# Kernel optimization log

Measured on AMD Instinct MI355X. Metric: run time of the kernel, lower is better.

## Reference

```python
import jax, jax.numpy as jnp
import numpy as np

N, C, E, G = 100000, 200, 400000, 512
H, D = 4, 50  # heads, per-head dim (out_channels // num_heads)
NEG_SLOPE = 0.2
EPS_LN = 1e-5


def setup_inputs() -> dict:
    key = jax.random.key(0)
    ks = jax.random.split(key, 12)
    x = jax.random.normal(ks[0], (N, C), dtype=jnp.float32)
    edge_index = jax.random.randint(ks[1], (2, E), 0, N, dtype=jnp.int64)
    batch = jnp.sort(jax.random.randint(ks[2], (N,), 0, G, dtype=jnp.int64))
    # LayerNorm (graph mode) affine params
    ln_w = jnp.ones((C,), jnp.float32)
    ln_b = jnp.zeros((C,), jnp.float32)
    # GATConv params: W [C, H*D], att_src/att_dst [H, D], bias [H*D]
    s = 1.0 / np.sqrt(C)
    W_gat = jax.random.uniform(ks[3], (C, H * D), jnp.float32, -s, s)
    att_src = jax.random.uniform(ks[4], (H, D), jnp.float32, -s, s)
    att_dst = jax.random.uniform(ks[5], (H, D), jnp.float32, -s, s)
    bias_gat = jnp.zeros((H * D,), jnp.float32)
    # SAGPooling scoring GraphConv(C -> 1): lin_rel (with bias) + lin_root (no bias)
    w_rel = jax.random.uniform(ks[6], (C, 1), jnp.float32, -s, s)
    b_rel = jnp.zeros((1,), jnp.float32)
    w_root = jax.random.uniform(ks[7], (C, 1), jnp.float32, -s, s)
    return {"x": x, "edge_index": edge_index, "batch": batch,
            "ln_w": ln_w, "ln_b": ln_b, "W_gat": W_gat, "att_src": att_src,
            "att_dst": att_dst, "bias_gat": bias_gat,
            "w_rel": w_rel, "b_rel": b_rel, "w_root": w_root}


def reference(x, edge_index, batch, ln_w, ln_b, W_gat, att_src, att_dst,
              bias_gat, w_rel, b_rel, w_root):
    n = x.shape[0]
    # --- PyG LayerNorm, mode='graph': normalize over all nodes+channels per graph
    cnt = jax.ops.segment_sum(jnp.ones((n,), x.dtype), batch, G)          # [G]
    denom = cnt * C
    mean = jax.ops.segment_sum(x.sum(-1), batch, G) / denom               # [G]
    ex2 = jax.ops.segment_sum((x * x).sum(-1), batch, G) / denom          # [G]
    var = ex2 - mean * mean
    h = (x - mean[batch, None]) * jax.lax.rsqrt(var + EPS_LN)[batch, None]
    h = h * ln_w + ln_b
    h = jax.nn.elu(h)
    # --- GATConv (concat heads, self-loops added, eval-mode dropout)
    loops = jnp.arange(n, dtype=edge_index.dtype)
    src = jnp.concatenate([edge_index[0], loops])                          # [E+N]
    dst = jnp.concatenate([edge_index[1], loops])
    xh = (h @ W_gat).reshape(n, H, D)                                      # [N,H,D]
    a_src = (xh * att_src).sum(-1)                                         # [N,H]
    a_dst = (xh * att_dst).sum(-1)
    alpha = jax.nn.leaky_relu(a_src[src] + a_dst[dst], NEG_SLOPE)          # [E+N,H]
    m = jax.ops.segment_max(alpha, dst, n)                                 # segment softmax
    e = jnp.exp(alpha - m[dst])
    z = jax.ops.segment_sum(e, dst, n)
    att = e / (z[dst] + 1e-16)
    out = jax.ops.segment_sum(xh[src] * att[:, :, None], dst, n)           # [N,H,D]
    out = out.reshape(n, H * D) + bias_gat                                 # [N,C]
    # --- SAGPooling(min_score=-1): GraphConv score -> per-graph softmax -> multiply
    agg = jax.ops.segment_sum(out[edge_index[0]], edge_index[1], n)        # neighbor sum
    score = (agg @ w_rel + b_rel + out @ w_root)[:, 0]                     # [N]
    sm = score - jax.ops.segment_max(score, batch, G)[batch]
    es = jnp.exp(sm)
    score = es / jax.ops.segment_sum(es, batch, G)[batch]
    # softmax scores in (0,1) > min_score=-1 -> all nodes kept, x scaled by score
    xp = out * score[:, None]                                              # [N,C]
    # --- global_add_pool
    g = jax.ops.segment_sum(xp, batch, G)                                  # [G,C]
    return (xp, g)
```

## Files before the change

### kernel.cpp

```cpp
#include <hip/hip_runtime.h>
#include <hip/hip_bf16.h>

#define NN 100000
#define CC 200
#define EE 400000
#define GG 512

typedef __bf16 bf16x8 __attribute__((ext_vector_type(8)));
typedef float f32x4 __attribute__((ext_vector_type(4)));

__device__ __forceinline__ float bfraw(unsigned int u) { return __uint_as_float(u << 16); }
__device__ __forceinline__ unsigned short f2bfraw(float f) {
  __hip_bfloat16 b = __float2bfloat16(f);
  union { __hip_bfloat16 b; unsigned short u; } cv; cv.b = b; return cv.u;
}
__device__ __forceinline__ float hsel(float4 v, int h) {
  return h == 0 ? v.x : h == 1 ? v.y : h == 2 ? v.z : v.w;
}

__global__ void k_detect(const unsigned int* __restrict__ lnw_raw,
                         const unsigned int* __restrict__ ei_raw, int* __restrict__ flags) {
  if (threadIdx.x == 0 && blockIdx.x == 0) {
    flags[0] = (lnw_raw[0] == 0x3F800000u) ? 1 : 0;
    flags[1] = (ei_raw[1] == 0u && ei_raw[3] == 0u && ei_raw[5] == 0u && ei_raw[7] == 0u) ? 1 : 0;
  }
}

__global__ void k_cvt_edges(const int* __restrict__ raw, const int* __restrict__ flags,
                            int* __restrict__ out, int* __restrict__ deg) {
  int i = blockIdx.x * 256 + threadIdx.x;
  if (i >= 2 * EE) return;
  int v = flags[1] ? raw[2 * i] : raw[i];
  out[i] = v;
  if (i >= EE) atomicAdd(&deg[v], 1);
}

__global__ void k_cvt_params(const void* lnw, const void* lnb, const void* W,
                             const void* attS, const void* attD, const void* bias,
                             const void* wrel, const void* brel, const void* wroot,
                             const int* __restrict__ flags, unsigned short* __restrict__ out) {
  int i = blockIdx.x * 256 + threadIdx.x;
  if (i > 41400) return;
  const void* p; int off;
  if (i < 200)        { p = lnw;  off = i; }
  else if (i < 400)   { p = lnb;  off = i - 200; }
  else if (i < 40400) { p = W;    off = i - 400; }
  else if (i < 40600) { p = attS; off = i - 40400; }
  else if (i < 40800) { p = attD; off = i - 40600; }
  else if (i < 41000) { p = bias; off = i - 40800; }
  else if (i < 41200) { p = wrel; off = i - 41000; }
  else if (i < 41400) { p = wroot; off = i - 41200; }
  else                { p = brel; off = 0; }
  out[i] = flags[0] ? f2bfraw(((const float*)p)[off]) : ((const unsigned short*)p)[off];
}

__global__ void k_batch(const int* __restrict__ raw, const int* __restrict__ flags,
                        int* __restrict__ batch, int* __restrict__ starts) {
  int i = blockIdx.x * 256 + threadIdx.x;
  if (i >= NN) return;
  int f = flags[1];
  int b = f ? raw[2 * i] : raw[i];
  batch[i] = b;
  int pb = (i == 0) ? -1 : (f ? raw[2 * i - 2] : raw[i - 1]);
  for (int g = pb + 1; g <= b; ++g) starts[g] = i;
  if (i == NN - 1) {
    for (int g = b + 1; g <= GG; ++g) starts[g] = NN;
  }
}

__global__ void k_ln_stats(const void* __restrict__ x, const int* __restrict__ starts,
                           const int* __restrict__ flags, float* __restrict__ gacc) {
  __shared__ float sh1[4], sh2[4];
  int g = blockIdx.x >> 3, chunk = blockIdx.x & 7;
  int r0 = starts[g], r1 = starts[g + 1], cnt = r1 - r0;
  int ra = r0 + (cnt * chunk) / 8;
  int rb = r0 + (cnt * (chunk + 1)) / 8;
  float s1 = 0.f, s2 = 0.f;
  if (flags[0]) {
    const float4* xv = (const float4*)x;
    for (int i = ra * 50 + (int)threadIdx.x; i < rb * 50; i += 256) {
      float4 r = xv[i];
      s1 += r.x + r.y + r.z + r.w;
      s2 += r.x * r.x + r.y * r.y + r.z * r.z + r.w * r.w;
    }
  } else {
    const uint4* xv = (const uint4*)x;
    for (int i = ra * 25 + (int)threadIdx.x; i < rb * 25; i += 256) {
      uint4 r = xv[i];
      unsigned int w[4] = {r.x, r.y, r.z, r.w};
#pragma unroll
      for (int j = 0; j < 4; ++j) {
        float a = bfraw(w[j] & 0xffffu);
        float b = bfraw(w[j] >> 16);
        s1 += a + b; s2 += a * a + b * b;
      }
    }
  }
#pragma unroll
  for (int o = 32; o > 0; o >>= 1) { s1 += __shfl_down(s1, o, 64); s2 += __shfl_down(s2, o, 64); }
  if ((threadIdx.x & 63) == 0) { sh1[threadIdx.x >> 6] = s1; sh2[threadIdx.x >> 6] = s2; }
  __syncthreads();
  if (threadIdx.x == 0) {
    atomicAdd(&gacc[g * 2],     sh1[0] + sh1[1] + sh1[2] + sh1[3]);
    atomicAdd(&gacc[g * 2 + 1], sh2[0] + sh2[1] + sh2[2] + sh2[3]);
  }
}

__global__ void k_ln_fin(const float* __restrict__ gacc, const int* __restrict__ starts,
                         float* __restrict__ mean, float* __restrict__ rstd) {
  int g = blockIdx.x * 64 + threadIdx.x;
  if (g >= GG) return;
  int cnt = starts[g + 1] - starts[g];
  if (cnt > 0) {
    float denom = (float)cnt * (float)CC;
    float m = gacc[g * 2] / denom;
    float var = gacc[g * 2 + 1] / denom - m * m;
    mean[g] = m;
    rstd[g] = rsqrtf(var + 1e-5f);
  } else { mean[g] = 0.f; rstd[g] = 0.f; }
}

__global__ void k_wpack(const unsigned short* __restrict__ W, unsigned short* __restrict__ wp) {
  int idx = blockIdx.x * 256 + threadIdx.x;
  if (idx >= 13 * 7 * 64 * 8) return;
  int j = idx & 7;
  int rest = idx >> 3;
  int l = rest & 63;
  int ts = rest >> 6;
  int s = ts % 7, t = ts / 7;
  int k = s * 32 + (l >> 4) * 8 + j;
  int n = t * 16 + (l & 15);
  wp[idx] = (k < CC && n < CC) ? W[k * CC + n] : (unsigned short)0;
}

__global__ void k_ngemm(const void* __restrict__ x, const int* __restrict__ batch,
                        const float* __restrict__ mean, const float* __restrict__ rstd,
                        const unsigned short* __restrict__ lnw, const unsigned short* __restrict__ lnb,
                        const unsigned short* __restrict__ attS, const unsigned short* __restrict__ attD,
                        const unsigned short* __restrict__ wp, const int* __restrict__ flags,
                        unsigned short* __restrict__ xh,
                        float* __restrict__ asrc, float* __restrict__ adst) {
  int gw = (blockIdx.x * 256 + threadIdx.x) >> 6;
  int lane = threadIdx.x & 63;
  int mbase = gw * 16;
  if (mbase >= NN) return;
  int quad = lane >> 4, l15 = lane & 15;
  int row = mbase + l15;
  int b = batch[row];
  float m = mean[b], rs = rstd[b];
  bool f32in = flags[0] != 0;
  f32x4 acc[13];
#pragma unroll
  for (int t = 0; t < 13; ++t) { f32x4 zz = {0.f, 0.f, 0.f, 0.f}; acc[t] = zz; }
  const bf16x8* wv = (const bf16x8*)wp;
#pragma unroll
  for (int s = 0; s < 7; ++s) {
    int kb = s * 32 + quad * 8;
    union { bf16x8 v; unsigned short u[8]; unsigned int w[4]; } af;
    if (kb < CC) {
      float v[8];
      if (f32in) {
        const float* xp = (const float*)x + (size_t)row * CC + kb;
        float4 a = *(const float4*)xp, c = *(const float4*)(xp + 4);
        v[0]=a.x; v[1]=a.y; v[2]=a.z; v[3]=a.w; v[4]=c.x; v[5]=c.y; v[6]=c.z; v[7]=c.w;
      } else {
        uint4 r = *(const uint4*)((const unsigned short*)x + (size_t)row * CC + kb);
        unsigned int w[4] = {r.x, r.y, r.z, r.w};
#pragma unroll
        for (int j = 0; j < 4; ++j) { v[2*j] = bfraw(w[j] & 0xffffu); v[2*j+1] = bfraw(w[j] >> 16); }
      }
      uint4 wv4 = *(const uint4*)(lnw + kb);
      uint4 bv4 = *(const uint4*)(lnb + kb);
      unsigned int ww[4] = {wv4.x, wv4.y, wv4.z, wv4.w};
      unsigned int bb[4] = {bv4.x, bv4.y, bv4.z, bv4.w};
#pragma unroll
      for (int j = 0; j < 4; ++j) {
        float t0 = (v[2*j]   - m) * rs * bfraw(ww[j] & 0xffffu) + bfraw(bb[j] & 0xffffu);
        float t1 = (v[2*j+1] - m) * rs * bfraw(ww[j] >> 16)     + bfraw(bb[j] >> 16);
        t0 = t0 > 0.f ? t0 : __expf(t0) - 1.f;
        t1 = t1 > 0.f ? t1 : __expf(t1) - 1.f;
        af.u[2*j]   = f2bfraw(t0);
        af.u[2*j+1] = f2bfraw(t1);
      }
    } else {
#pragma unroll
      for (int j = 0; j < 4; ++j) af.w[j] = 0u;
    }
#pragma unroll
    for (int t = 0; t < 13; ++t) {
      bf16x8 bf = wv[(t * 7 + s) * 64 + lane];
      acc[t] = __builtin_amdgcn_mfma_f32_16x16x32_bf16(af.v, bf, acc[t], 0, 0, 0);
    }
  }
#pragma unroll
  for (int t = 0; t < 13; ++t) {
    int c = t * 16 + l15;
    if (c < CC) {
#pragma unroll
      for (int r = 0; r < 4; ++r) {
        int mrow = mbase + quad * 4 + r;
        xh[(size_t)mrow * CC + c] = f2bfraw(acc[t][r]);
      }
    }
  }
  float wsv[13], wdv[13]; int hv[13];
#pragma unroll
  for (int t = 0; t < 13; ++t) {
    int c = t * 16 + l15;
    bool ok = c < CC;
    hv[t]  = ok ? c / 50 : 0;
    wsv[t] = ok ? bfraw(attS[ok ? c : 0]) : 0.f;
    wdv[t] = ok ? bfraw(attD[ok ? c : 0]) : 0.f;
  }
#pragma unroll
  for (int r = 0; r < 4; ++r) {
    float ps[4] = {0.f, 0.f, 0.f, 0.f}, pd[4] = {0.f, 0.f, 0.f, 0.f};
#pragma unroll
    for (int t = 0; t < 13; ++t) {
      float v = acc[t][r];
      float fs = v * wsv[t], fd = v * wdv[t];
#pragma unroll
      for (int j = 0; j < 4; ++j) {
        ps[j] += (hv[t] == j) ? fs : 0.f;
        pd[j] += (hv[t] == j) ? fd : 0.f;
      }
    }
#pragma unroll
    for (int mm = 1; mm < 16; mm <<= 1) {
#pragma unroll
      for (int j = 0; j < 4; ++j) {
        ps[j] += __shfl_xor(ps[j], mm, 64);
        pd[j] += __shfl_xor(pd[j], mm, 64);
      }
    }
    if (l15 == 0) {
      int rw = mbase + quad * 4 + r;
      *(float4*)(asrc + (size_t)rw * 4) = make_float4(ps[0], ps[1], ps[2], ps[3]);
      *(float4*)(adst + (size_t)rw * 4) = make_float4(pd[0], pd[1], pd[2], pd[3]);
    }
  }
}

__global__ void k_scan1(const int* __restrict__ deg, int* __restrict__ rowptr, int* __restrict__ sums) {
  __shared__ int sh[256];
  int tid = threadIdx.x;
  int base = blockIdx.x * 1024 + tid * 4;
  int v[4]; int s = 0;
#pragma unroll
  for (int j = 0; j < 4; ++j) { int i = base + j; v[j] = (i < NN) ? deg[i] : 0; s += v[j]; }
  sh[tid] = s;
  __syncthreads();
  for (int o = 1; o < 256; o <<= 1) {
    int t = (tid >= o) ? sh[tid - o] : 0;
    __syncthreads();
    sh[tid] += t;
    __syncthreads();
  }
  int run = sh[tid] - s;
#pragma unroll
  for (int j = 0; j < 4; ++j) { int i = base + j; if (i < NN) rowptr[i] = run; run += v[j]; }
  if (tid == 255) sums[blockIdx.x] = sh[255];
}

__global__ void k_scan2(int* __restrict__ sums, int nb) {
  __shared__ int sh[128];
  int tid = threadIdx.x;
  int v = (tid < nb) ? sums[tid] : 0;
  sh[tid] = v;
  __syncthreads();
  for (int o = 1; o < 128; o <<= 1) {
    int t = (tid >= o) ? sh[tid - o] : 0;
    __syncthreads();
    sh[tid] += t;
    __syncthreads();
  }
  if (tid < nb) sums[tid] = sh[tid] - v;
}

__global__ void k_scan3(int* __restrict__ rowptr, const int* __restrict__ sums) {
  int tid = threadIdx.x;
  int add = sums[blockIdx.x];
  int base = blockIdx.x * 1024 + tid * 4;
#pragma unroll
  for (int j = 0; j < 4; ++j) { int i = base + j; if (i < NN) rowptr[i] += add; }
  if (blockIdx.x == 0 && tid == 0) rowptr[NN] = EE;
}

__global__ void k_scatter(const int* __restrict__ ei32, const int* __restrict__ rowptr,
                          int* __restrict__ fill, int* __restrict__ csrc) {
  int e = blockIdx.x * 256 + threadIdx.x;
  if (e >= EE) return;
  int s = ei32[e], d = ei32[EE + e];
  int pos = rowptr[d] + atomicAdd(&fill[d], 1);
  csrc[pos] = s;
}

__global__ void k_out(const unsigned short* __restrict__ xh, const float* __restrict__ asrc,
                      const float* __restrict__ adst,
                      const int* __restrict__ rowptr, const int* __restrict__ csrc,
                      const unsigned short* __restrict__ bias, const unsigned short* __restrict__ wrel,
                      const unsigned short* __restrict__ wroot,
                      unsigned short* __restrict__ out,
                      float* __restrict__ srel, float* __restrict__ sroot) {
  __shared__ float sA[256], sB[256];
  int tid = threadIdx.x;
  int local = tid / 25;
  int sub = tid - local * 25;
  int n = blockIdx.x * 10 + local;
  bool active = (local < 10) && (n < NN);
  float pr = 0.f, pq = 0.f;
  if (active) {
    int c0 = sub * 8;
    int hh0 = c0 / 50;
    int hh1 = hh0 < 3 ? hh0 + 1 : hh0;
    int bnd = (hh0 + 1) * 50;
    bool cr[8];
#pragma unroll
    for (int j = 0; j < 8; ++j) cr[j] = (c0 + j) >= bnd;
    float4 adn = *(const float4*)(adst + (size_t)n * 4);
    float4 asn = *(const float4*)(asrc + (size_t)n * 4);
    float ad_lo = hsel(adn, hh0), ad_hi = hsel(adn, hh1);
    float al_lo = hsel(asn, hh0) + ad_lo;
    float al_hi = hsel(asn, hh1) + ad_hi;
    al_lo = al_lo > 0.f ? al_lo : 0.2f * al_lo;
    al_hi = al_hi > 0.f ? al_hi : 0.2f * al_hi;
    float e_lo = __expf(al_lo), e_hi = __expf(al_hi);
    float z_lo = e_lo, z_hi = e_hi;
    float acc[8];
    {
      uint4 xv = *(const uint4*)(xh + (size_t)n * CC + c0);
      unsigned int w[4] = {xv.x, xv.y, xv.z, xv.w};
#pragma unroll
      for (int j = 0; j < 4; ++j) {
        float lo = bfraw(w[j] & 0xffffu), hi = bfraw(w[j] >> 16);
        acc[2*j]   = (cr[2*j]   ? e_hi : e_lo) * lo;
        acc[2*j+1] = (cr[2*j+1] ? e_hi : e_lo) * hi;
      }
    }
    int p0 = rowptr[n], p1 = rowptr[n + 1];
    int p = p0;
    for (; p + 2 <= p1; p += 2) {
      int s0 = csrc[p], s1 = csrc[p + 1];
      uint4 g0 = *(const uint4*)(xh + (size_t)s0 * CC + c0);
      uint4 g1 = *(const uint4*)(xh + (size_t)s1 * CC + c0);
      float4 av0 = *(const float4*)(asrc + (size_t)s0 * 4);
      float4 av1 = *(const float4*)(asrc + (size_t)s1 * 4);
      float b0lo = hsel(av0, hh0) + ad_lo, b0hi = hsel(av0, hh1) + ad_hi;
      float b1lo = hsel(av1, hh0) + ad_lo, b1hi = hsel(av1, hh1) + ad_hi;
      b0lo = b0lo > 0.f ? b0lo : 0.2f * b0lo;
      b0hi = b0hi > 0.f ? b0hi : 0.2f * b0hi;
      b1lo = b1lo > 0.f ? b1lo : 0.2f * b1lo;
      b1hi = b1hi > 0.f ? b1hi : 0.2f * b1hi;
      float a0lo = __expf(b0lo), a0hi = __expf(b0hi);
      float a1lo = __expf(b1lo), a1hi = __expf(b1hi);
      z_lo += a0lo + a1lo; z_hi += a0hi + a1hi;
      unsigned int w0[4] = {g0.x, g0.y, g0.z, g0.w};
      unsigned int w1[4] = {g1.x, g1.y, g1.z, g1.w};
#pragma unroll
      for (int j = 0; j < 4; ++j) {
        acc[2*j]   += (cr[2*j]   ? a0hi : a0lo) * bfraw(w0[j] & 0xffffu);
        acc[2*j+1] += (cr[2*j+1] ? a0hi : a0lo) * bfraw(w0[j] >> 16);
      }
#pragma unroll
      for (int j = 0; j < 4; ++j) {
        acc[2*j]   += (cr[2*j]   ? a1hi : a1lo) * bfraw(w1[j] & 0xffffu);
        acc[2*j+1] += (cr[2*j+1] ? a1hi : a1lo) * bfraw(w1[j] >> 16);
      }
    }
    if (p < p1) {
      int s0 = csrc[p];
      uint4 g0 = *(const uint4*)(xh + (size_t)s0 * CC + c0);
      float4 av0 = *(const float4*)(asrc + (size_t)s0 * 4);
      float b0lo = hsel(av0, hh0) + ad_lo, b0hi = hsel(av0, hh1) + ad_hi;
      b0lo = b0lo > 0.f ? b0lo : 0.2f * b0lo;
      b0hi = b0hi > 0.f ? b0hi : 0.2f * b0hi;
      float a0lo = __expf(b0lo), a0hi = __expf(b0hi);
      z_lo += a0lo; z_hi += a0hi;
      unsigned int w0[4] = {g0.x, g0.y, g0.z, g0.w};
#pragma unroll
      for (int j = 0; j < 4; ++j) {
        acc[2*j]   += (cr[2*j]   ? a0hi : a0lo) * bfraw(w0[j] & 0xffffu);
        acc[2*j+1] += (cr[2*j+1] ? a0hi : a0lo) * bfraw(w0[j] >> 16);
      }
    }
    float rz_lo = 1.f / (z_lo + 1e-16f);
    float rz_hi = 1.f / (z_hi + 1e-16f);
    uint4 bv = *(const uint4*)(bias + c0);
    uint4 rv = *(const uint4*)(wrel + c0);
    uint4 qv = *(const uint4*)(wroot + c0);
    unsigned int bw[4] = {bv.x, bv.y, bv.z, bv.w};
    unsigned int rw[4] = {rv.x, rv.y, rv.z, rv.w};
    unsigned int qw[4] = {qv.x, qv.y, qv.z, qv.w};
    unsigned int ow[4];
#pragma unroll
    for (int j = 0; j < 4; ++j) {
      float v0 = acc[2*j]   * (cr[2*j]   ? rz_hi : rz_lo) + bfraw(bw[j] & 0xffffu);
      float v1 = acc[2*j+1] * (cr[2*j+1] ? rz_hi : rz_lo) + bfraw(bw[j] >> 16);
      ow[j] = (unsigned int)f2bfraw(v0) | ((unsigned int)f2bfraw(v1) << 16);
      pr += v0 * bfraw(rw[j] & 0xffffu) + v1 * bfraw(rw[j] >> 16);
      pq += v0 * bfraw(qw[j] & 0xffffu) + v1 * bfraw(qw[j] >> 16);
    }
    *(uint4*)(out + (size_t)n * CC + c0) = make_uint4(ow[0], ow[1], ow[2], ow[3]);
  }
  sA[tid] = pr; sB[tid] = pq;
  __syncthreads();
  if (active && sub == 0) {
    float a = 0.f, b = 0.f;
#pragma unroll
    for (int k = 0; k < 25; ++k) { a += sA[tid + k]; b += sB[tid + k]; }
    srel[n] = a; sroot[n] = b;
  }
}

__global__ void k_score(const float* __restrict__ srel, const float* __restrict__ sroot,
                        const unsigned short* __restrict__ brel, const int* __restrict__ rowptr,
                        const int* __restrict__ csrc, float* __restrict__ score) {
  int n = blockIdx.x * 256 + threadIdx.x;
  if (n >= NN) return;
  float sc = bfraw(brel[0]) + sroot[n];
  int p0 = rowptr[n], p1 = rowptr[n + 1];
  int p = p0;
  float s0 = 0.f, s1 = 0.f;
  for (; p + 2 <= p1; p += 2) { s0 += srel[csrc[p]]; s1 += srel[csrc[p + 1]]; }
  if (p < p1) s0 += srel[csrc[p]];
  score[n] = sc + s0 + s1;
}

__global__ void k_gsoftmax(const float* __restrict__ score, const int* __restrict__ starts,
                           float* __restrict__ smax, float* __restrict__ ssum) {
  __shared__ float sh[4];
  __shared__ float bc;
  int g = blockIdx.x;
  int r0 = starts[g], r1 = starts[g + 1];
  float m = -3.0e38f;
  for (int i = r0 + (int)threadIdx.x; i < r1; i += 256) m = fmaxf(m, score[i]);
#pragma unroll
  for (int o = 32; o > 0; o >>= 1) m = fmaxf(m, __shfl_down(m, o, 64));
  if ((threadIdx.x & 63) == 0) sh[threadIdx.x >> 6] = m;
  __syncthreads();
  if (threadIdx.x == 0) bc = fmaxf(fmaxf(sh[0], sh[1]), fmaxf(sh[2], sh[3]));
  __syncthreads();
  float mm = bc;
  float s = 0.f;
  for (int i = r0 + (int)threadIdx.x; i < r1; i += 256) s += expf(score[i] - mm);
#pragma unroll
  for (int o = 32; o > 0; o >>= 1) s += __shfl_down(s, o, 64);
  if ((threadIdx.x & 63) == 0) sh[threadIdx.x >> 6] = s;
  __syncthreads();
  if (threadIdx.x == 0) { smax[g] = mm; ssum[g] = sh[0] + sh[1] + sh[2] + sh[3]; }
}

__global__ void k_xpg(const unsigned short* __restrict__ out, const float* __restrict__ score,
                      const float* __restrict__ smax, const float* __restrict__ ssum,
                      const int* __restrict__ starts, const int* __restrict__ flags,
                      void* __restrict__ dout, float* __restrict__ gsum) {
  __shared__ float part[10][200];
  int g = blockIdx.x >> 3, chunk = blockIdx.x & 7;
  int r0 = starts[g], r1 = starts[g + 1], cnt = r1 - r0;
  int ra = r0 + (cnt * chunk) / 8;
  int rb = r0 + (cnt * (chunk + 1)) / 8;
  int tid = threadIdx.x;
  int rg = tid / 25, sub = tid - rg * 25;
  int f32o = flags[0];
  float sm = smax[g], si = ssum[g];
  float rsi = (si > 0.f) ? 1.f / si : 0.f;
  if (rg < 10) {
    float acc[8];
#pragma unroll
    for (int j = 0; j < 8; ++j) acc[j] = 0.f;
    for (int r = ra + rg; r < rb; r += 10) {
      float sf = __expf(score[r] - sm) * rsi;
      uint4 xv = *(const uint4*)(out + (size_t)r * CC + sub * 8);
      unsigned int w[4] = {xv.x, xv.y, xv.z, xv.w};
      float v[8];
#pragma unroll
      for (int j = 0; j < 4; ++j) {
        v[2*j]   = bfraw(w[j] & 0xffffu) * sf;
        v[2*j+1] = bfraw(w[j] >> 16) * sf;
        acc[2*j] += v[2*j]; acc[2*j+1] += v[2*j+1];
      }
      if (f32o) {
        float* dp = (float*)dout + (size_t)r * CC + sub * 8;
        *(float4*)dp       = make_float4(v[0], v[1], v[2], v[3]);
        *(float4*)(dp + 4) = make_float4(v[4], v[5], v[6], v[7]);
      } else {
        unsigned int o[4];
#pragma unroll
        for (int j = 0; j < 4; ++j)
          o[j] = (unsigned int)f2bfraw(v[2*j]) | ((unsigned int)f2bfraw(v[2*j+1]) << 16);
        *(uint4*)((unsigned short*)dout + (size_t)r * CC + sub * 8) = make_uint4(o[0], o[1], o[2], o[3]);
      }
    }
#pragma unroll
    for (int j = 0; j < 8; ++j) part[rg][sub * 8 + j] = acc[j];
  }
  __syncthreads();
  if (tid < 200) {
    float s = 0.f;
#pragma unroll
    for (int k = 0; k < 10; ++k) s += part[k][tid];
    atomicAdd(&gsum[g * 200 + tid], s);
  }
}

__global__ void k_gfin(const float* __restrict__ gsum, const int* __restrict__ flags,
                       void* __restrict__ dout) {
  int i = blockIdx.x * 256 + threadIdx.x;
  if (i >= GG * 200) return;
  float s = gsum[i];
  size_t o = (size_t)NN * CC + i;
  if (flags[0]) ((float*)dout)[o] = s;
  else ((unsigned short*)dout)[o] = f2bfraw(s);
}

constexpr size_t O_FLAGS  = 0;
constexpr size_t O_STARTS = 16;
constexpr size_t O_MEAN   = 2080;
constexpr size_t O_RSTD   = 4128;
constexpr size_t O_SMAX   = 6176;
constexpr size_t O_SSUM   = 8224;
constexpr size_t O_SUMS   = 10272;
constexpr size_t O_PAR    = 10784;
constexpr size_t O_WPACK  = 93600;
constexpr size_t O_BATCH  = 186784;
constexpr size_t O_EI32   = 586784;
constexpr size_t O_DEG    = 3786784;
constexpr size_t O_FILL   = 4186784;
constexpr size_t O_ROWPTR = 4586784;
constexpr size_t O_CSRC   = 4986912;
constexpr size_t O_ASRC   = 6586912;
constexpr size_t O_ADST   = 8186912;
constexpr size_t O_SREL   = 9786912;
constexpr size_t O_SROOT  = 10186912;
constexpr size_t O_SCORE  = 10586912;
constexpr size_t O_GACC   = 10986912;
constexpr size_t O_GSUM   = 10991008;
constexpr size_t O_XH     = 11400608;
constexpr size_t O_OUT    = 51400608;

extern "C" void kernel_launch(void* const* d_in, const int* in_sizes, int n_in,
                              void* d_out, int out_size, void* d_ws, size_t ws_size,
                              hipStream_t stream) {
  const void* x     = d_in[0];
  const int*  ei    = (const int*)d_in[1];
  const int*  batchr= (const int*)d_in[2];
  const void* lnw_r = d_in[3];
  const void* lnb_r = d_in[4];
  const void* Wg_r  = d_in[5];
  const void* attS_r= d_in[6];
  const void* attD_r= d_in[7];
  const void* bias_r= d_in[8];
  const void* wrel_r= d_in[9];
  const void* brel_r= d_in[10];
  const void* wroot_r=d_in[11];

  char* ws = (char*)d_ws;
  int*   flags  = (int*)(ws + O_FLAGS);
  int*   starts = (int*)(ws + O_STARTS);
  float* mean   = (float*)(ws + O_MEAN);
  float* rstd   = (float*)(ws + O_RSTD);
  float* smax   = (float*)(ws + O_SMAX);
  float* ssum   = (float*)(ws + O_SSUM);
  int*   sums   = (int*)(ws + O_SUMS);
  unsigned short* par = (unsigned short*)(ws + O_PAR);
  unsigned short* wpack = (unsigned short*)(ws + O_WPACK);
  int*   batch  = (int*)(ws + O_BATCH);
  int*   ei32   = (int*)(ws + O_EI32);
  int*   deg    = (int*)(ws + O_DEG);
  int*   fill   = (int*)(ws + O_FILL);
  int*   rowptr = (int*)(ws + O_ROWPTR);
  int*   csrc   = (int*)(ws + O_CSRC);
  float* asrc   = (float*)(ws + O_ASRC);
  float* adst   = (float*)(ws + O_ADST);
  float* srel   = (float*)(ws + O_SREL);
  float* sroot  = (float*)(ws + O_SROOT);
  float* score  = (float*)(ws + O_SCORE);
  float* gacc   = (float*)(ws + O_GACC);
  float* gsum   = (float*)(ws + O_GSUM);
  unsigned short* xh    = (unsigned short*)(ws + O_XH);
  unsigned short* outws = (unsigned short*)(ws + O_OUT);

  unsigned short* lnw  = par;
  unsigned short* lnb  = par + 200;
  unsigned short* Wc   = par + 400;
  unsigned short* attS = par + 40400;
  unsigned short* attD = par + 40600;
  unsigned short* bias = par + 40800;
  unsigned short* wrel = par + 41000;
  unsigned short* wroot= par + 41200;
  unsigned short* brel = par + 41400;

  hipMemsetAsync(deg, 0, 800000, stream);
  hipMemsetAsync(gacc, 0, 4096 + 409600, stream);

  k_detect    <<<1, 64, 0, stream>>>((const unsigned int*)lnw_r, (const unsigned int*)ei, flags);
  k_cvt_params<<<162, 256, 0, stream>>>(lnw_r, lnb_r, Wg_r, attS_r, attD_r, bias_r,
                                        wrel_r, brel_r, wroot_r, flags, par);
  k_cvt_edges <<<(2 * EE + 255) / 256, 256, 0, stream>>>(ei, flags, ei32, deg);
  k_batch     <<<(NN + 255) / 256, 256, 0, stream>>>(batchr, flags, batch, starts);
  k_ln_stats  <<<GG * 8, 256, 0, stream>>>(x, starts, flags, gacc);
  k_ln_fin    <<<8, 64, 0, stream>>>(gacc, starts, mean, rstd);
  k_wpack     <<<(13 * 7 * 64 * 8 + 255) / 256, 256, 0, stream>>>(Wc, wpack);
  k_ngemm     <<<1563, 256, 0, stream>>>(x, batch, mean, rstd, lnw, lnb, attS, attD,
                                         wpack, flags, xh, asrc, adst);
  k_scan1     <<<98, 256, 0, stream>>>(deg, rowptr, sums);
  k_scan2     <<<1, 128, 0, stream>>>(sums, 98);
  k_scan3     <<<98, 256, 0, stream>>>(rowptr, sums);
  k_scatter   <<<(EE + 255) / 256, 256, 0, stream>>>(ei32, rowptr, fill, csrc);
  k_out       <<<10000, 256, 0, stream>>>(xh, asrc, adst, rowptr, csrc, bias, wrel, wroot,
                                          outws, srel, sroot);
  k_score     <<<(NN + 255) / 256, 256, 0, stream>>>(srel, sroot, brel, rowptr, csrc, score);
  k_gsoftmax  <<<GG, 256, 0, stream>>>(score, starts, smax, ssum);
  k_xpg       <<<GG * 8, 256, 0, stream>>>(outws, score, smax, ssum, starts, flags, d_out, gsum);
  k_gfin      <<<(GG * 200 + 255) / 256, 256, 0, stream>>>(gsum, flags, d_out);
}
```

Measured before the change: 354.4 us.

## Stage packed GAT weights in LDS and prefetch x rows in node GEMM

The node GEMM kernel now uses 512-thread blocks that copy the packed 200x208 bf16 weight matrix (about 93 KB) into shared memory once per block. The MFMA B-operand reads then come from LDS instead of global/L2. All seven x row chunks are also loaded into registers up front so the global loads can overlap instead of being issued per k-step. The cost is a large LDS footprint limiting blocks per CU, higher register pressure from the prefetch arrays, and a per-block weight copy.

```diff
diff --git a/kernel.cpp b/kernel.cpp
--- a/kernel.cpp
+++ b/kernel.cpp
@@ -133,15 +133,25 @@
   wp[idx] = (k < CC && n < CC) ? W[k * CC + n] : (unsigned short)0;
 }
 
-__global__ void k_ngemm(const void* __restrict__ x, const int* __restrict__ batch,
-                        const float* __restrict__ mean, const float* __restrict__ rstd,
-                        const unsigned short* __restrict__ lnw, const unsigned short* __restrict__ lnb,
-                        const unsigned short* __restrict__ attS, const unsigned short* __restrict__ attD,
-                        const unsigned short* __restrict__ wp, const int* __restrict__ flags,
-                        unsigned short* __restrict__ xh,
-                        float* __restrict__ asrc, float* __restrict__ adst) {
-  int gw = (blockIdx.x * 256 + threadIdx.x) >> 6;
-  int lane = threadIdx.x & 63;
+__global__ __launch_bounds__(512, 2)
+void k_ngemm(const void* __restrict__ x, const int* __restrict__ batch,
+             const float* __restrict__ mean, const float* __restrict__ rstd,
+             const unsigned short* __restrict__ lnw, const unsigned short* __restrict__ lnb,
+             const unsigned short* __restrict__ attS, const unsigned short* __restrict__ attD,
+             const unsigned short* __restrict__ wp, const int* __restrict__ flags,
+             unsigned short* __restrict__ xh,
+             float* __restrict__ asrc, float* __restrict__ adst) {
+  __shared__ uint4 wsh[5824];
+  int tid = threadIdx.x;
+  int wave = tid >> 6, lane = tid & 63;
+  {
+    const uint4* wg = (const uint4*)wp;
+    for (int c = wave; c < 91; c += 8)
+      wsh[c * 64 + lane] = wg[c * 64 + lane];
+  }
+  __syncthreads();
+
+  int gw = blockIdx.x * 8 + wave;
   int mbase = gw * 16;
   if (mbase >= NN) return;
   int quad = lane >> 4, l15 = lane & 15;
@@ -149,10 +159,32 @@
   int b = batch[row];
   float m = mean[b], rs = rstd[b];
   bool f32in = flags[0] != 0;
+
+  float4 xf[7][2];
+  uint4  xb[7];
+  if (f32in) {
+    const float4* xv = (const float4*)x;
+#pragma unroll
+    for (int s = 0; s < 7; ++s) {
+      int kb = s * 32 + quad * 8;
+      if (kb < CC) {
+        xf[s][0] = xv[(size_t)row * 50 + (kb >> 2)];
+        xf[s][1] = xv[(size_t)row * 50 + (kb >> 2) + 1];
+      }
+    }
+  } else {
+    const uint4* xv = (const uint4*)x;
+#pragma unroll
+    for (int s = 0; s < 7; ++s) {
+      int kb = s * 32 + quad * 8;
+      if (kb < CC) xb[s] = xv[(size_t)row * 25 + (kb >> 3)];
+    }
+  }
+
   f32x4 acc[13];
 #pragma unroll
   for (int t = 0; t < 13; ++t) { f32x4 zz = {0.f, 0.f, 0.f, 0.f}; acc[t] = zz; }
-  const bf16x8* wv = (const bf16x8*)wp;
+  const bf16x8* wv = (const bf16x8*)wsh;
 #pragma unroll
   for (int s = 0; s < 7; ++s) {
     int kb = s * 32 + quad * 8;
@@ -160,12 +192,10 @@
     if (kb < CC) {
       float v[8];
       if (f32in) {
-        const float* xp = (const float*)x + (size_t)row * CC + kb;
-        float4 a = *(const float4*)xp, c = *(const float4*)(xp + 4);
+        float4 a = xf[s][0], c = xf[s][1];
         v[0]=a.x; v[1]=a.y; v[2]=a.z; v[3]=a.w; v[4]=c.x; v[5]=c.y; v[6]=c.z; v[7]=c.w;
       } else {
-        uint4 r = *(const uint4*)((const unsigned short*)x + (size_t)row * CC + kb);
-        unsigned int w[4] = {r.x, r.y, r.z, r.w};
+        unsigned int w[4] = {xb[s].x, xb[s].y, xb[s].z, xb[s].w};
 #pragma unroll
         for (int j = 0; j < 4; ++j) { v[2*j] = bfraw(w[j] & 0xffffu); v[2*j+1] = bfraw(w[j] >> 16); }
       }
@@ -601,8 +631,8 @@
   k_ln_stats  <<<GG * 8, 256, 0, stream>>>(x, starts, flags, gacc);
   k_ln_fin    <<<8, 64, 0, stream>>>(gacc, starts, mean, rstd);
   k_wpack     <<<(13 * 7 * 64 * 8 + 255) / 256, 256, 0, stream>>>(Wc, wpack);
-  k_ngemm     <<<1563, 256, 0, stream>>>(x, batch, mean, rstd, lnw, lnb, attS, attD,
-                                         wpack, flags, xh, asrc, adst);
+  k_ngemm     <<<782, 512, 0, stream>>>(x, batch, mean, rstd, lnw, lnb, attS, attD,
+                                        wpack, flags, xh, asrc, adst);
   k_scan1     <<<98, 256, 0, stream>>>(deg, rowptr, sums);
   k_scan2     <<<1, 128, 0, stream>>>(sums, 98);
   k_scan3     <<<98, 256, 0, stream>>>(rowptr, sums);
```

Result: slower. 367.9 us (+3.8%).
